# Kernel optimization log

Measured on AMD Instinct MI355X. Metric: run time of the kernel, lower is better.

## Reference

```python
import jax, jax.numpy as jnp
from jax import lax
import numpy as np

EMBED = 20
FILTERS = 16
KSIZES = (1, 3, 5, 7, 9)
LIN_IN = 7 * len(KSIZES) * FILTERS  # 560
LIN_DIM = 64
SEQ_LENS = {'pep': 12, 'a1': 7, 'a2': 8, 'a3': 16, 'b1': 6, 'b2': 7, 'b3': 18}
BATCH = 16384


def setup_inputs() -> dict:
    key = jax.random.key(0)
    keys = jax.random.split(key, 16)
    inp = {}
    for i, (name, L) in enumerate(SEQ_LENS.items()):
        inp[name] = jax.random.normal(keys[i], (BATCH, EMBED, L), dtype=jnp.float32)
    # Conv weights: one stacked array per kernel size, [7 sequences, FILTERS, EMBED, k]
    for j, k in enumerate(KSIZES):
        inp[f'Wk{k}'] = jax.random.normal(keys[7 + j], (7, FILTERS, EMBED, k), dtype=jnp.float32) * 0.1
    inp['lin1_w'] = jax.random.normal(keys[12], (LIN_DIM, LIN_IN), dtype=jnp.float32) * 0.05
    inp['lin1_b'] = jnp.zeros((LIN_DIM,), dtype=jnp.float32)
    inp['lin2_w'] = jax.random.normal(keys[13], (1, LIN_DIM), dtype=jnp.float32) * 0.1
    inp['lin2_b'] = jnp.zeros((1,), dtype=jnp.float32)
    return inp


def _conv_relu_gmax(x, w):
    # x: [B, C, L], w: [F, C, k] -> SAME conv + ReLU + global max over length -> [B, F]
    y = lax.conv_general_dilated(x, w, window_strides=(1,), padding='SAME',
                                 dimension_numbers=('NCH', 'OIH', 'NCH'))
    return jnp.max(jax.nn.relu(y), axis=-1)


def _branch(x, ws):
    # x scaled by 1/5 as in the torch forward; concat pooled features over kernel sizes
    x = x / 5.0
    return jnp.concatenate([_conv_relu_gmax(x, w) for w in ws], axis=1)  # [B, 5*F]


def reference(pep, a1, a2, a3, b1, b2, b3, Wk1, Wk3, Wk5, Wk7, Wk9,
              lin1_w, lin1_b, lin2_w, lin2_b):
    seqs = [pep, a1, a2, a3, b1, b2, b3]
    Wks = [Wk1, Wk3, Wk5, Wk7, Wk9]
    feats = jnp.concatenate(
        [_branch(seqs[i], [W[i] for W in Wks]) for i in range(7)], axis=1)  # [B, 560]
    # Dropout is identity at inference.
    h = jax.nn.sigmoid(feats @ lin1_w.T + lin1_b)  # [B, 64]
    out = h @ lin2_w.T + lin2_b                    # [B, 1]
    return out.reshape(-1)                          # [B]
```

## Files before the change

kernel.cpp:

```cpp
#include <hip/hip_runtime.h>
#include <stdint.h>
#include <stddef.h>

typedef short bfrag __attribute__((ext_vector_type(8)));
typedef float f32x4 __attribute__((ext_vector_type(4)));

#define NSEQ 7

__constant__ int c_ks[5] = {1, 3, 5, 7, 9};

#define SLO0 3
#define SLO1 2
#define SLO2 1
#define SLO3 0
#define SLO4 0
#define SN0 1
#define SN1 3
#define SN2 5
#define SN3 6
#define SN4 7

static __device__ __forceinline__ unsigned short f2bf(float f) {
  unsigned int u = __float_as_uint(f);
  u += 0x7FFFu + ((u >> 16) & 1u);
  return (unsigned short)(u >> 16);
}

struct PrepArgs {
  const float* Wk[5];
  const float* lin1_w;
  bfrag* Wpack;
  bfrag* lin1pack;
};

__global__ __launch_bounds__(256) void prep_kernel(PrepArgs a) {
  int tid = blockIdx.x * 256 + threadIdx.x;
  const int NW = NSEQ * 5 * 7 * 64;
  if (tid < NW) {
    int lane = tid & 63, rest = tid >> 6;
    int step = rest % 7, nt = (rest / 7) % 5, seq = rest / 35;
    int quad = lane >> 4, f = lane & 15;
    int ks = c_ks[nt], off = (9 - ks) >> 1;
    const float* W = a.Wk[nt];
    bfrag s;
#pragma unroll
    for (int j = 0; j < 8; ++j) {
      int k = step * 32 + quad * 8 + j;
      int t = k / 24, c = k % 24;
      int tap = t - off;
      float val = 0.f;
      if (c < 20 && tap >= 0 && tap < ks)
        val = W[((seq * 16 + f) * 20 + c) * ks + tap] * 0.2f;
      s[j] = (short)f2bf(val);
    }
    a.Wpack[tid] = s;
  } else if (tid < NW + 4 * 18 * 64) {
    int t2 = tid - NW;
    int lane = t2 & 63, rest = t2 >> 6;
    int step = rest % 18, nt = rest / 18;
    int quad = lane >> 4, col = lane & 15;
    int n = nt * 16 + col;
    bfrag s;
#pragma unroll
    for (int j = 0; j < 8; ++j) {
      int k = step * 32 + quad * 8 + j;
      float val = (k < 560) ? a.lin1_w[n * 560 + k] : 0.f;
      s[j] = (short)f2bf(val);
    }
    a.lin1pack[t2] = s;
  }
}

struct ConvArgs {
  const float* x[NSEQ];
  const bfrag* Wpack;
  unsigned short* feats;
};

static __device__ __forceinline__ void store_feat(unsigned short* feats, int b, int k, float v) {
  int step = k >> 5, q = (k >> 3) & 3, j = k & 7;
  feats[((size_t)(b >> 4) * 18 + step) * 512 + (q * 16 + (b & 15)) * 8 + j] = f2bf(v);
}

template <int Lc, int SHIFTc, int MTc, int TBBv, int Pv>
__device__ __forceinline__ void conv_body(unsigned short* xl, const ConvArgs& a,
                                          const int seq, const int b0) {
  const int tid = threadIdx.x;
  const float* xg = a.x[seq];

  for (int i = tid; i < TBBv * Pv * 24 / 8; i += 256) ((uint4*)xl)[i] = uint4{0, 0, 0, 0};
  __syncthreads();
  for (int r = tid; r < TBBv * 20; r += 256) {
    int b = r / 20, c = r % 20;
    const float* src = xg + ((size_t)(b0 + b) * 20 + c) * Lc;
    unsigned short* dst = xl + (b * Pv + 4) * 24 + c;
#pragma unroll
    for (int xi = 0; xi < Lc; ++xi) dst[xi * 24] = f2bf(src[xi]);
  }
  __syncthreads();

  const int wave = tid >> 6, lane = tid & 63, quad = lane >> 4, m = lane & 15;

  const bfrag* wp = a.Wpack + (size_t)(seq * 5 * 7) * 64 + lane;
  bfrag Bf[22];
  {
    int bi = 0;
#pragma unroll
    for (int i = 0; i < SN0; ++i) Bf[bi++] = wp[(0 * 7 + SLO0 + i) * 64];
#pragma unroll
    for (int i = 0; i < SN1; ++i) Bf[bi++] = wp[(1 * 7 + SLO1 + i) * 64];
#pragma unroll
    for (int i = 0; i < SN2; ++i) Bf[bi++] = wp[(2 * 7 + SLO2 + i) * 64];
#pragma unroll
    for (int i = 0; i < SN3; ++i) Bf[bi++] = wp[(3 * 7 + SLO3 + i) * 64];
#pragma unroll
    for (int i = 0; i < SN4; ++i) Bf[bi++] = wp[(4 * 7 + SLO4 + i) * 64];
  }
#pragma unroll
  for (int i = 0; i < 22; ++i) __asm__ volatile("" : "+v"(Bf[i]));

  constexpr int njobs = (MTc == 2) ? TBBv : ((TBBv << SHIFTc) >> 4);
  constexpr int bpt = (MTc == 1 && SHIFTc == 3) ? 2 : 1;
  constexpr int lmask = (1 << SHIFTc) - 1;

  for (int job = wave; job < njobs; job += 4) {
    float v0 = 0.f, v1 = 0.f, v2 = 0.f, v3 = 0.f, v4 = 0.f;
#pragma unroll
    for (int sub = 0; sub < MTc; ++sub) {
      int bl, l;
      if (MTc == 2) { bl = job; l = sub * 2 + m; }
      else { int r = job * 16 + m; bl = r >> SHIFTc; l = r & lmask; }
      const unsigned short* arow = &xl[(bl * Pv + l) * 24 + quad * 8];
      f32x4 acc0 = {0.f, 0.f, 0.f, 0.f}, acc1 = acc0, acc2 = acc0, acc3 = acc0, acc4 = acc0;
#pragma unroll
      for (int s = 0; s < 7; ++s) {
        bfrag Af = *(const bfrag*)(arow + s * 32);
        if (s >= SLO0 && s < SLO0 + SN0)
          acc0 = __builtin_amdgcn_mfma_f32_16x16x32_bf16(Af, Bf[0 + s - SLO0], acc0, 0, 0, 0);
        if (s >= SLO1 && s < SLO1 + SN1)
          acc1 = __builtin_amdgcn_mfma_f32_16x16x32_bf16(Af, Bf[1 + s - SLO1], acc1, 0, 0, 0);
        if (s >= SLO2 && s < SLO2 + SN2)
          acc2 = __builtin_amdgcn_mfma_f32_16x16x32_bf16(Af, Bf[4 + s - SLO2], acc2, 0, 0, 0);
        if (s >= SLO3 && s < SLO3 + SN3)
          acc3 = __builtin_amdgcn_mfma_f32_16x16x32_bf16(Af, Bf[9 + s - SLO3], acc3, 0, 0, 0);
        acc4 = __builtin_amdgcn_mfma_f32_16x16x32_bf16(Af, Bf[15 + s], acc4, 0, 0, 0);
      }
#pragma unroll
      for (int r4 = 0; r4 < 4; ++r4) {
        bool ok = (MTc == 2) ? true : (((quad * 4 + r4) & lmask) < Lc);
        v0 = fmaxf(v0, ok ? acc0[r4] : 0.f);
        v1 = fmaxf(v1, ok ? acc1[r4] : 0.f);
        v2 = fmaxf(v2, ok ? acc2[r4] : 0.f);
        v3 = fmaxf(v3, ok ? acc3[r4] : 0.f);
        v4 = fmaxf(v4, ok ? acc4[r4] : 0.f);
      }
    }
    v0 = fmaxf(v0, __shfl_xor(v0, 16));
    v1 = fmaxf(v1, __shfl_xor(v1, 16));
    v2 = fmaxf(v2, __shfl_xor(v2, 16));
    v3 = fmaxf(v3, __shfl_xor(v3, 16));
    v4 = fmaxf(v4, __shfl_xor(v4, 16));
    if (bpt == 1) {
      v0 = fmaxf(v0, __shfl_xor(v0, 32));
      v1 = fmaxf(v1, __shfl_xor(v1, 32));
      v2 = fmaxf(v2, __shfl_xor(v2, 32));
      v3 = fmaxf(v3, __shfl_xor(v3, 32));
      v4 = fmaxf(v4, __shfl_xor(v4, 32));
      if (lane < 16) {
        int b = b0 + job, kb = seq * 80 + lane;
        store_feat(a.feats, b, kb, v0);      store_feat(a.feats, b, kb + 16, v1);
        store_feat(a.feats, b, kb + 32, v2); store_feat(a.feats, b, kb + 48, v3);
        store_feat(a.feats, b, kb + 64, v4);
      }
    } else {
      if ((lane & 16) == 0) {
        int b = b0 + job * 2 + (lane >> 5), kb = seq * 80 + (lane & 15);
        store_feat(a.feats, b, kb, v0);      store_feat(a.feats, b, kb + 16, v1);
        store_feat(a.feats, b, kb + 32, v2); store_feat(a.feats, b, kb + 48, v3);
        store_feat(a.feats, b, kb + 64, v4);
      }
    }
  }
}

__global__ __launch_bounds__(256, 3) void conv_kernel(ConvArgs a) {
  __shared__ __align__(16) unsigned short xl[32 * 25 * 24];
  const int bid = blockIdx.x;
  if (bid < 3072) {
    const int seq = bid >> 9, b0 = (bid & 511) * 32;
    switch (seq) {
      case 0: conv_body<12, 4, 1, 32, 25>(xl, a, 0, b0); break;
      case 1: conv_body< 7, 3, 1, 32, 25>(xl, a, 1, b0); break;
      case 2: conv_body< 8, 3, 1, 32, 25>(xl, a, 2, b0); break;
      case 3: conv_body<16, 4, 1, 32, 25>(xl, a, 3, b0); break;
      case 4: conv_body< 6, 3, 1, 32, 25>(xl, a, 4, b0); break;
      default: conv_body< 7, 3, 1, 32, 25>(xl, a, 5, b0); break;
    }
  } else {
    conv_body<18, 5, 2, 16, 41>(xl, a, 6, (bid - 3072) * 16);
  }
}

struct MlpArgs {
  const bfrag* feats;
  const bfrag* lin1pack;
  const float* lin1_b;
  const float* lin2_w;
  const float* lin2_b;
  float* out;
};

__global__ __launch_bounds__(256, 4) void mlp_kernel(MlpArgs a) {
  __shared__ float h[16 * 68];
  __shared__ float w2[64];
  const int tid = threadIdx.x;
  const int b0 = blockIdx.x * 16;
  if (tid < 64) w2[tid] = a.lin2_w[tid];
  const int wave = tid >> 6, lane = tid & 63, quad = lane >> 4, m = lane & 15;
  const int nt = wave;
  bfrag Bf[18];
#pragma unroll
  for (int s = 0; s < 18; ++s) Bf[s] = a.lin1pack[(nt * 18 + s) * 64 + lane];
#pragma unroll
  for (int s = 0; s < 18; ++s) __asm__ volatile("" : "+v"(Bf[s]));
  const bfrag* ap = a.feats + (size_t)blockIdx.x * 18 * 64 + lane;
  f32x4 acc = {0.f, 0.f, 0.f, 0.f};
#pragma unroll
  for (int s = 0; s < 18; ++s)
    acc = __builtin_amdgcn_mfma_f32_16x16x32_bf16(ap[s * 64], Bf[s], acc, 0, 0, 0);
  int n = nt * 16 + m;
  float bias = a.lin1_b[n];
#pragma unroll
  for (int r = 0; r < 4; ++r) {
    float pre = acc[r] + bias;
    h[(quad * 4 + r) * 68 + n] = 1.f / (1.f + __expf(-pre));
  }
  __syncthreads();
  int bl = tid >> 4, q = tid & 15;
  const float* hr = &h[bl * 68 + q * 4];
  float s = hr[0] * w2[q * 4] + hr[1] * w2[q * 4 + 1] + hr[2] * w2[q * 4 + 2] + hr[3] * w2[q * 4 + 3];
  s += __shfl_xor(s, 1);
  s += __shfl_xor(s, 2);
  s += __shfl_xor(s, 4);
  s += __shfl_xor(s, 8);
  if (q == 0) a.out[b0 + bl] = s + a.lin2_b[0];
}

extern "C" void kernel_launch(void* const* d_in, const int* in_sizes, int n_in,
                              void* d_out, int out_size, void* d_ws, size_t ws_size,
                              hipStream_t stream) {
  (void)in_sizes; (void)n_in; (void)out_size; (void)ws_size;
  char* ws = (char*)d_ws;
  bfrag* Wpack = (bfrag*)(ws + 0);
  bfrag* lin1pack = (bfrag*)(ws + 262144);
  unsigned short* feats = (unsigned short*)(ws + 393216);

  PrepArgs pa;
  for (int j = 0; j < 5; ++j) pa.Wk[j] = (const float*)d_in[7 + j];
  pa.lin1_w = (const float*)d_in[12];
  pa.Wpack = Wpack;
  pa.lin1pack = lin1pack;
  prep_kernel<<<80, 256, 0, stream>>>(pa);

  ConvArgs ca;
  for (int i = 0; i < NSEQ; ++i) ca.x[i] = (const float*)d_in[i];
  ca.Wpack = Wpack;
  ca.feats = feats;
  conv_kernel<<<4096, 256, 0, stream>>>(ca);

  MlpArgs ma;
  ma.feats = (const bfrag*)feats;
  ma.lin1pack = lin1pack;
  ma.lin1_b = (const float*)d_in[13];
  ma.lin2_w = (const float*)d_in[14];
  ma.lin2_b = (const float*)d_in[15];
  ma.out = (float*)d_out;
  mlp_kernel<<<1024, 256, 0, stream>>>(ma);
}
```

Measured before the change: 186.9 us.

## Skip padded conv rows and split seq6 into main tile plus partial tail

```diff
diff --git a/kernel.cpp b/kernel.cpp
--- a/kernel.cpp
+++ b/kernel.cpp
@@ -20,6 +20,10 @@
 #define SN3 6
 #define SN4 7
 
+#define XL_HW 22016
+#define ZOFF 19200
+#define PART_OFF 19456
+
 static __device__ __forceinline__ unsigned short f2bf(float f) {
   unsigned int u = __float_as_uint(f);
   u += 0x7FFFu + ((u >> 16) & 1u);
@@ -82,13 +86,34 @@
   feats[((size_t)(b >> 4) * 18 + step) * 512 + (q * 16 + (b & 15)) * 8 + j] = f2bf(v);
 }
 
-template <int Lc, int SHIFTc, int MTc, int TBBv, int Pv>
+template <int SLO, int SN>
+static __device__ __forceinline__ void mfma_group(f32x4& acc, int s, const bfrag& Af,
+                                                  const bfrag* BfBase) {
+  if (s >= SLO && s < SLO + SN)
+    acc = __builtin_amdgcn_mfma_f32_16x16x32_bf16(Af, BfBase[s - SLO], acc, 0, 0, 0);
+}
+
+static __device__ __forceinline__ void tile_mfma(const unsigned short* arow, const bfrag* Bf,
+                                                 f32x4 acc[5]) {
+#pragma unroll
+  for (int s = 0; s < 7; ++s) {
+    bfrag Af = *(const bfrag*)(arow + s * 32);
+    mfma_group<SLO0, SN0>(acc[0], s, Af, Bf + 0);
+    mfma_group<SLO1, SN1>(acc[1], s, Af, Bf + 1);
+    mfma_group<SLO2, SN2>(acc[2], s, Af, Bf + 4);
+    mfma_group<SLO3, SN3>(acc[3], s, Af, Bf + 9);
+    acc[4] = __builtin_amdgcn_mfma_f32_16x16x32_bf16(Af, Bf[15 + s], acc[4], 0, 0, 0);
+  }
+}
+
+template <int Lc, int SHIFTc, int SEQ6c, int TBBv, int Pv>
 __device__ __forceinline__ void conv_body(unsigned short* xl, const ConvArgs& a,
                                           const int seq, const int b0) {
   const int tid = threadIdx.x;
   const float* xg = a.x[seq];
 
-  for (int i = tid; i < TBBv * Pv * 24 / 8; i += 256) ((uint4*)xl)[i] = uint4{0, 0, 0, 0};
+  constexpr int ZWORDS = (SEQ6c ? TBBv * Pv * 24 : ZOFF + 256) / 8;
+  for (int i = tid; i < ZWORDS; i += 256) ((uint4*)xl)[i] = uint4{0, 0, 0, 0};
   __syncthreads();
   for (int r = tid; r < TBBv * 20; r += 256) {
     int b = r / 20, c = r % 20;
@@ -116,45 +141,49 @@
 #pragma unroll
     for (int i = 0; i < SN4; ++i) Bf[bi++] = wp[(4 * 7 + SLO4 + i) * 64];
   }
-#pragma unroll
-  for (int i = 0; i < 22; ++i) __asm__ volatile("" : "+v"(Bf[i]));
-
-  constexpr int njobs = (MTc == 2) ? TBBv : ((TBBv << SHIFTc) >> 4);
-  constexpr int bpt = (MTc == 1 && SHIFTc == 3) ? 2 : 1;
+
+  float* part = (float*)(xl + PART_OFF);
+
+  if (SEQ6c) {
+    if (wave < 2) {
+      int bl = wave * 8 + (m >> 1), l = 16 + (m & 1);
+      const unsigned short* arow = &xl[(bl * Pv + l) * 24 + quad * 8];
+      f32x4 acc[5];
+#pragma unroll
+      for (int g = 0; g < 5; ++g) acc[g] = f32x4{0.f, 0.f, 0.f, 0.f};
+      tile_mfma(arow, Bf, acc);
+#pragma unroll
+      for (int g = 0; g < 5; ++g) {
+        float p0 = fmaxf(fmaxf(acc[g][0], acc[g][1]), 0.f);
+        float p1 = fmaxf(fmaxf(acc[g][2], acc[g][3]), 0.f);
+        part[(wave * 8 + 2 * quad) * 80 + g * 16 + m] = p0;
+        part[(wave * 8 + 2 * quad + 1) * 80 + g * 16 + m] = p1;
+      }
+    }
+    __syncthreads();
+  }
+
+  constexpr int njobs = SEQ6c ? TBBv : ((TBBv << SHIFTc) >> 4);
+  constexpr int bpt = (!SEQ6c && SHIFTc == 3) ? 2 : 1;
   constexpr int lmask = (1 << SHIFTc) - 1;
 
   for (int job = wave; job < njobs; job += 4) {
-    float v0 = 0.f, v1 = 0.f, v2 = 0.f, v3 = 0.f, v4 = 0.f;
-#pragma unroll
-    for (int sub = 0; sub < MTc; ++sub) {
-      int bl, l;
-      if (MTc == 2) { bl = job; l = sub * 2 + m; }
-      else { int r = job * 16 + m; bl = r >> SHIFTc; l = r & lmask; }
-      const unsigned short* arow = &xl[(bl * Pv + l) * 24 + quad * 8];
-      f32x4 acc0 = {0.f, 0.f, 0.f, 0.f}, acc1 = acc0, acc2 = acc0, acc3 = acc0, acc4 = acc0;
-#pragma unroll
-      for (int s = 0; s < 7; ++s) {
-        bfrag Af = *(const bfrag*)(arow + s * 32);
-        if (s >= SLO0 && s < SLO0 + SN0)
-          acc0 = __builtin_amdgcn_mfma_f32_16x16x32_bf16(Af, Bf[0 + s - SLO0], acc0, 0, 0, 0);
-        if (s >= SLO1 && s < SLO1 + SN1)
-          acc1 = __builtin_amdgcn_mfma_f32_16x16x32_bf16(Af, Bf[1 + s - SLO1], acc1, 0, 0, 0);
-        if (s >= SLO2 && s < SLO2 + SN2)
-          acc2 = __builtin_amdgcn_mfma_f32_16x16x32_bf16(Af, Bf[4 + s - SLO2], acc2, 0, 0, 0);
-        if (s >= SLO3 && s < SLO3 + SN3)
-          acc3 = __builtin_amdgcn_mfma_f32_16x16x32_bf16(Af, Bf[9 + s - SLO3], acc3, 0, 0, 0);
-        acc4 = __builtin_amdgcn_mfma_f32_16x16x32_bf16(Af, Bf[15 + s], acc4, 0, 0, 0);
-      }
-#pragma unroll
-      for (int r4 = 0; r4 < 4; ++r4) {
-        bool ok = (MTc == 2) ? true : (((quad * 4 + r4) & lmask) < Lc);
-        v0 = fmaxf(v0, ok ? acc0[r4] : 0.f);
-        v1 = fmaxf(v1, ok ? acc1[r4] : 0.f);
-        v2 = fmaxf(v2, ok ? acc2[r4] : 0.f);
-        v3 = fmaxf(v3, ok ? acc3[r4] : 0.f);
-        v4 = fmaxf(v4, ok ? acc4[r4] : 0.f);
-      }
-    }
+    int bl, l;
+    if (SEQ6c) { bl = job; l = m; }
+    else { int r = job * 16 + m; bl = r >> SHIFTc; l = r & lmask; }
+    const unsigned short* arow = (SEQ6c || l < Lc)
+        ? &xl[(bl * Pv + l) * 24 + quad * 8]
+        : &xl[ZOFF + quad * 8];
+    f32x4 acc[5];
+#pragma unroll
+    for (int g = 0; g < 5; ++g) acc[g] = f32x4{0.f, 0.f, 0.f, 0.f};
+    tile_mfma(arow, Bf, acc);
+
+    float v0 = fmaxf(fmaxf(fmaxf(acc[0][0], acc[0][1]), fmaxf(acc[0][2], acc[0][3])), 0.f);
+    float v1 = fmaxf(fmaxf(fmaxf(acc[1][0], acc[1][1]), fmaxf(acc[1][2], acc[1][3])), 0.f);
+    float v2 = fmaxf(fmaxf(fmaxf(acc[2][0], acc[2][1]), fmaxf(acc[2][2], acc[2][3])), 0.f);
+    float v3 = fmaxf(fmaxf(fmaxf(acc[3][0], acc[3][1]), fmaxf(acc[3][2], acc[3][3])), 0.f);
+    float v4 = fmaxf(fmaxf(fmaxf(acc[4][0], acc[4][1]), fmaxf(acc[4][2], acc[4][3])), 0.f);
     v0 = fmaxf(v0, __shfl_xor(v0, 16));
     v1 = fmaxf(v1, __shfl_xor(v1, 16));
     v2 = fmaxf(v2, __shfl_xor(v2, 16));
@@ -167,6 +196,13 @@
       v3 = fmaxf(v3, __shfl_xor(v3, 32));
       v4 = fmaxf(v4, __shfl_xor(v4, 32));
       if (lane < 16) {
+        if (SEQ6c) {
+          v0 = fmaxf(v0, part[job * 80 + 0 + lane]);
+          v1 = fmaxf(v1, part[job * 80 + 16 + lane]);
+          v2 = fmaxf(v2, part[job * 80 + 32 + lane]);
+          v3 = fmaxf(v3, part[job * 80 + 48 + lane]);
+          v4 = fmaxf(v4, part[job * 80 + 64 + lane]);
+        }
         int b = b0 + job, kb = seq * 80 + lane;
         store_feat(a.feats, b, kb, v0);      store_feat(a.feats, b, kb + 16, v1);
         store_feat(a.feats, b, kb + 32, v2); store_feat(a.feats, b, kb + 48, v3);
@@ -184,20 +220,20 @@
 }
 
 __global__ __launch_bounds__(256, 3) void conv_kernel(ConvArgs a) {
-  __shared__ __align__(16) unsigned short xl[32 * 25 * 24];
+  __shared__ __align__(16) unsigned short xl[XL_HW];
   const int bid = blockIdx.x;
   if (bid < 3072) {
     const int seq = bid >> 9, b0 = (bid & 511) * 32;
     switch (seq) {
-      case 0: conv_body<12, 4, 1, 32, 25>(xl, a, 0, b0); break;
-      case 1: conv_body< 7, 3, 1, 32, 25>(xl, a, 1, b0); break;
-      case 2: conv_body< 8, 3, 1, 32, 25>(xl, a, 2, b0); break;
-      case 3: conv_body<16, 4, 1, 32, 25>(xl, a, 3, b0); break;
-      case 4: conv_body< 6, 3, 1, 32, 25>(xl, a, 4, b0); break;
-      default: conv_body< 7, 3, 1, 32, 25>(xl, a, 5, b0); break;
+      case 0: conv_body<12, 4, 0, 32, 25>(xl, a, 0, b0); break;
+      case 1: conv_body< 7, 3, 0, 32, 25>(xl, a, 1, b0); break;
+      case 2: conv_body< 8, 3, 0, 32, 25>(xl, a, 2, b0); break;
+      case 3: conv_body<16, 4, 0, 32, 25>(xl, a, 3, b0); break;
+      case 4: conv_body< 6, 3, 0, 32, 25>(xl, a, 4, b0); break;
+      default: conv_body< 7, 3, 0, 32, 25>(xl, a, 5, b0); break;
     }
   } else {
-    conv_body<18, 5, 2, 16, 41>(xl, a, 6, (bid - 3072) * 16);
+    conv_body<18, 5, 1, 16, 41>(xl, a, 6, (bid - 3072) * 16);
   }
 }
 
@@ -221,8 +257,6 @@
   bfrag Bf[18];
 #pragma unroll
   for (int s = 0; s < 18; ++s) Bf[s] = a.lin1pack[(nt * 18 + s) * 64 + lane];
-#pragma unroll
-  for (int s = 0; s < 18; ++s) __asm__ volatile("" : "+v"(Bf[s]));
   const bfrag* ap = a.feats + (size_t)blockIdx.x * 18 * 64 + lane;
   f32x4 acc = {0.f, 0.f, 0.f, 0.f};
 #pragma unroll
```

Measured after the change: 182.1 us. 2.5% less time.
